# Performance work log

Measured on AMD Instinct MI355X. Metric: run time of the kernel, lower is better.

## Reference

```python
import jax, jax.numpy as jnp
import numpy as np

HEAD_DIM = 128
NUM_Q_HEAD = 32
NUM_KV_HEAD = 8
GROUP_SIZE = 128
EPS = 1e-5
WINDOW = 512
CAP = 50.0
CLIP_L, CLIP_R = -0.01, 1.01
SCALE = 1.0 / np.sqrt(HEAD_DIM)
NEG = -1e9


def group_rmsnorm(x, gamma, gsz, eps):
    # x: [B, S, H]; per-group RMS over contiguous chunks of size gsz, then learned scale
    b, s, h = x.shape
    xg = x.reshape(b, s, h // gsz, gsz)
    rms = jnp.sqrt(jnp.mean(xg * xg, axis=-1, keepdims=True) + eps)
    return (xg / rms).reshape(b, s, h) * gamma


def setup_inputs() -> dict:
    key = jax.random.key(0)
    k1, k2, k3, k4, k5 = jax.random.split(key, 5)
    B, S = 2, 2048
    q = jax.random.normal(k1, (B, S, NUM_Q_HEAD, HEAD_DIM), dtype=jnp.float32)
    k = jax.random.normal(k2, (B, S, NUM_KV_HEAD, HEAD_DIM), dtype=jnp.float32)
    v = jax.random.normal(k3, (B, S, NUM_KV_HEAD, HEAD_DIM), dtype=jnp.float32)
    # GroupRMSNorm weights ~ U(init_range) = U(-1, 1)
    gamma_q = jax.random.uniform(k4, (NUM_Q_HEAD * HEAD_DIM,), dtype=jnp.float32, minval=-1.0, maxval=1.0)
    gamma_k = jax.random.uniform(k5, (NUM_KV_HEAD * HEAD_DIM,), dtype=jnp.float32, minval=-1.0, maxval=1.0)
    return {"q": q, "k": k, "v": v, "gamma_q": gamma_q, "gamma_k": gamma_k}


def reference(q, k, v, gamma_q, gamma_k):
    B, Sq, Hq, D = q.shape
    Sk, Hkv = k.shape[1], k.shape[2]
    # QK GroupRMSNorm on flattened hidden dim
    qn = group_rmsnorm(q.reshape(B, Sq, Hq * D), gamma_q, GROUP_SIZE, EPS).reshape(B, Sq, Hq, D)
    kn = group_rmsnorm(k.reshape(B, Sk, Hkv * D), gamma_k, GROUP_SIZE, EPS).reshape(B, Sk, Hkv, D)
    # GQA: repeat_interleave kv heads to match q heads
    rep = Hq // Hkv
    kr = jnp.repeat(kn, rep, axis=2)
    vr = jnp.repeat(v, rep, axis=2)
    # scores: [B, H, Sq, Sk]
    logits = jnp.einsum('bqhd,bkhd->bhqk', qn, kr) * SCALE
    # softmax capping (temperature path skipped when cap is set)
    logits = jnp.tanh(logits / CAP) * CAP
    # causal + sliding-window mask (aligned at sequence end)
    i = jnp.arange(Sq)[:, None]
    j = jnp.arange(Sk)[None, :]
    pos = i + (Sk - Sq)
    allowed = (j <= pos) & (pos - j <= WINDOW)
    logits = jnp.where(allowed, logits, NEG)
    probs = jax.nn.softmax(logits.astype(jnp.float32), axis=-1)
    # softmax clipping: clamp(probs * (r - l) + l, 0, 1)
    probs = jnp.clip(probs * (CLIP_R - CLIP_L) + CLIP_L, 0.0, 1.0)
    # output: [B, Sq, H, D]
    o = jnp.einsum('bhqk,bkhd->bqhd', probs.astype(q.dtype), vr)
    return o
```

## Files before the change

kernel.cpp:

```cpp
#include <hip/hip_runtime.h>

#define SEQ     2048
#define NQH     32
#define NKV     8
#define HD      128
#define WINDOW  512
#define QT      64
#define EPS_F   1e-5f
#define CQ2     0.12752981793f
#define PSTR    72

#define KN_OFF  0ull
#define VT_OFF  8388608ull

#define ROWPAT(r, hg) ((((r) & 3) + 8 * ((r) >> 2)) + 4 * (hg))

#define ASYNC_BAR() asm volatile("s_waitcnt vmcnt(0)\n\ts_barrier" ::: "memory")
#define LGKM_BAR()  asm volatile("s_waitcnt lgkmcnt(0)\n\ts_barrier" ::: "memory")

using bf16x8 = __attribute__((ext_vector_type(8))) __bf16;
using f32x16 = __attribute__((ext_vector_type(16))) float;

__device__ __forceinline__ void dma16(const void* g, void* l) {
    __builtin_amdgcn_global_load_lds(
        (const __attribute__((address_space(1))) unsigned int*)g,
        (__attribute__((address_space(3))) unsigned int*)l, 16, 0, 0);
}

__global__ __launch_bounds__(256)
void prep(const float* __restrict__ k, const float* __restrict__ v,
          const float* __restrict__ gk,
          __bf16* __restrict__ kn, __bf16* __restrict__ vt)
{
    __shared__ __align__(16) __bf16 sT[HD * 72];
    const int blk = blockIdx.x;
    const int tid = threadIdx.x;
    if (blk < 512) {
        const int l16  = tid & 15;
        const int rsub = tid >> 4;
        #pragma unroll
        for (int it = 0; it < 4; it++) {
            const int row = blk * 64 + it * 16 + rsub;
            const float* src = k + (size_t)row * HD + l16 * 8;
            const float* g   = gk + (row & 7) * HD + l16 * 8;
            float4 a  = *(const float4*)(src);
            float4 b4 = *(const float4*)(src + 4);
            float ss = a.x*a.x + a.y*a.y + a.z*a.z + a.w*a.w
                     + b4.x*b4.x + b4.y*b4.y + b4.z*b4.z + b4.w*b4.w;
            ss += __shfl_xor(ss, 1); ss += __shfl_xor(ss, 2);
            ss += __shfl_xor(ss, 4); ss += __shfl_xor(ss, 8);
            const float rs = rsqrtf(ss * (1.f / 128.f) + EPS_F);
            float4 g0 = *(const float4*)(g);
            float4 g1 = *(const float4*)(g + 4);
            bf16x8 o;
            o[0] = (__bf16)(a.x  * rs * g0.x);  o[1] = (__bf16)(a.y  * rs * g0.y);
            o[2] = (__bf16)(a.z  * rs * g0.z);  o[3] = (__bf16)(a.w  * rs * g0.w);
            o[4] = (__bf16)(b4.x * rs * g1.x);  o[5] = (__bf16)(b4.y * rs * g1.y);
            o[6] = (__bf16)(b4.z * rs * g1.z);  o[7] = (__bf16)(b4.w * rs * g1.w);
            *(bf16x8*)(kn + (size_t)row * HD + l16 * 8) = o;
        }
    } else {
        const int blk2 = blk - 512;
        const int st  = blk2 & 31;
        const int kvh = (blk2 >> 5) & 7;
        const int b   = blk2 >> 8;
        const int s0  = st * 64;
        {
            const int r  = tid >> 2;
            const int q4 = tid & 3;
            const float* src = v + ((size_t)(b * SEQ + s0 + r) * NKV + kvh) * HD;
            #pragma unroll
            for (int u = 0; u < 8; u++) {
                const int d0 = q4 * 4 + u * 16;
                float4 x = *(const float4*)(src + d0);
                sT[(d0 + 0) * 72 + r] = (__bf16)x.x;
                sT[(d0 + 1) * 72 + r] = (__bf16)x.y;
                sT[(d0 + 2) * 72 + r] = (__bf16)x.z;
                sT[(d0 + 3) * 72 + r] = (__bf16)x.w;
            }
        }
        __syncthreads();
        {
            const int c     = tid & 7;
            const int dbase = tid >> 3;
            __bf16* dst = vt + ((size_t)(b * NKV + kvh) * HD) * SEQ + s0;
            #pragma unroll
            for (int i = 0; i < 4; i++) {
                const int d = dbase + i * 32;
                bf16x8 w = *(const bf16x8*)&sT[d * 72 + c * 8];
                *(bf16x8*)(dst + (size_t)d * SEQ + c * 8) = w;
            }
        }
    }
}

__global__ __launch_bounds__(256, 2)
void swa_main(const float* __restrict__ q, const __bf16* __restrict__ kn,
              const __bf16* __restrict__ vt, const float* __restrict__ gq,
              float* __restrict__ out)
{
    __shared__ __align__(16) __bf16 sKV[2][QT * HD];
    __shared__ __align__(16) __bf16 sP[QT * PSTR];
    __shared__ float sLp[2][QT];
    __shared__ float sInvL[QT];

    const int wg   = blockIdx.x;
    const int qt   = wg & 31;
    const int h    = (wg >> 5) & 31;
    const int b    = wg >> 10;
    const int kvh  = h >> 2;
    const int i0   = qt * QT;
    const int tid  = threadIdx.x;
    const int lane = tid & 63;
    const int wave = tid >> 6;
    const int mhalf = wave & 1;
    const int nhalf = wave >> 1;
    const int m    = lane & 31;
    const int hg   = lane >> 5;

    const char* k_src[4];  const char* v_src[4];
    int kq_off[4];  int v_off[4];
    {
        const char* kn_head = (const char*)kn + ((size_t)b * SEQ * NKV + kvh) * 256;
        const char* vt_head = (const char*)vt + ((size_t)(b * NKV + kvh) * HD) * (SEQ * 2);
        #pragma unroll
        for (int i = 0; i < 4; i++) {
            const int chunk = wave * 4 + i;
            {
                const int r    = chunk * 4 + (lane >> 4);
                const int cpos = lane & 15;
                const int c    = (cpos & 8) | ((cpos ^ r) & 7);
                k_src[i]  = kn_head + (size_t)r * (NKV * HD * 2) + c * 16;
                kq_off[i] = chunk * 1024;
            }
            {
                const int r    = chunk * 8 + (lane >> 3);
                const int cpos = lane & 7;
                const int c    = cpos ^ (r & 7);
                v_src[i] = vt_head + (size_t)r * (SEQ * 2) + c * 16;
                v_off[i] = chunk * 1024;
            }
        }
    }

    const int t_lo   = (i0 >= WINDOW ? (i0 - WINDOW) : 0) >> 6;
    const int t_hi   = i0 >> 6;
    const int ttbias = t_hi - 8;
    const int krow   = nhalf * 32 + m;

    {
        const size_t ko = (size_t)t_lo * 64 * (NKV * HD * 2);
        const int p0 = (t_lo - ttbias) & 1;
        #pragma unroll
        for (int i = 0; i < 4; i++) dma16(k_src[i] + ko, (char*)&sKV[p0][0] + kq_off[i]);
    }

    bf16x8 qf[8];
    {
        const int qrow = i0 + mhalf * 32 + m;
        const float* qp = q + ((size_t)(b * SEQ + qrow) * NQH + h) * HD;
        float4 qb[16];
        float ss = 0.0f;
        #pragma unroll
        for (int kf = 0; kf < 8; kf++) {
            const int d0 = kf * 16 + hg * 8;
            float4 a  = *(const float4*)(qp + d0);
            float4 b4 = *(const float4*)(qp + d0 + 4);
            qb[kf * 2] = a; qb[kf * 2 + 1] = b4;
            ss += a.x*a.x + a.y*a.y + a.z*a.z + a.w*a.w
                + b4.x*b4.x + b4.y*b4.y + b4.z*b4.z + b4.w*b4.w;
        }
        ss += __shfl_xor(ss, 32);
        const float rs = rsqrtf(ss * (1.f / 128.f) + EPS_F) * CQ2;
        const float* gp = gq + h * HD;
        #pragma unroll
        for (int kf = 0; kf < 8; kf++) {
            const int d0 = kf * 16 + hg * 8;
            float4 g0 = *(const float4*)(gp + d0);
            float4 g1 = *(const float4*)(gp + d0 + 4);
            bf16x8 f;
            f[0] = (__bf16)(qb[kf*2].x   * rs * g0.x);
            f[1] = (__bf16)(qb[kf*2].y   * rs * g0.y);
            f[2] = (__bf16)(qb[kf*2].z   * rs * g0.z);
            f[3] = (__bf16)(qb[kf*2].w   * rs * g0.w);
            f[4] = (__bf16)(qb[kf*2+1].x * rs * g1.x);
            f[5] = (__bf16)(qb[kf*2+1].y * rs * g1.y);
            f[6] = (__bf16)(qb[kf*2+1].z * rs * g1.z);
            f[7] = (__bf16)(qb[kf*2+1].w * rs * g1.w);
            qf[kf] = f;
        }
    }

    float lacc[16];
    #pragma unroll
    for (int i = 0; i < 16; i++) lacc[i] = 0.f;
    bf16x8 ec[9][2];

    #pragma unroll
    for (int tt = 0; tt < 9; tt++) {
        const int t = ttbias + tt;
        if (t >= t_lo) {
            ASYNC_BAR();
            const __bf16* kb = &sKV[tt & 1][0];
            bf16x8 bk[8];
            #pragma unroll
            for (int kf = 0; kf < 8; kf++) {
                const int cc  = kf * 2 + hg;
                const int pos = (cc & 8) | ((cc ^ krow) & 7);
                bk[kf] = *(const bf16x8*)(kb + krow * HD + pos * 8);
            }
            if (t < t_hi) {
                const size_t ko = (size_t)(t + 1) * 64 * (NKV * HD * 2);
                #pragma unroll
                for (int i = 0; i < 4; i++)
                    dma16(k_src[i] + ko, (char*)&sKV[(tt + 1) & 1][0] + kq_off[i]);
            }
            f32x16 c;
            #pragma unroll
            for (int i = 0; i < 16; i++) c[i] = 0.f;
            #pragma unroll
            for (int kf = 0; kf < 8; kf++)
                c = __builtin_amdgcn_mfma_f32_32x32x16_bf16(qf[kf], bk[kf], c, 0, 0, 0);

            const bool do_mask = (t == t_hi) || (t == t_lo && i0 >= WINDOW);
            const int kj = t * 64 + krow;
            float e[16];
            #pragma unroll
            for (int r = 0; r < 16; r++) {
                float ev = __builtin_amdgcn_exp2f(c[r]);
                if (do_mask) {
                    const int qi = i0 + mhalf * 32 + ROWPAT(r, hg);
                    ev = ((unsigned)(qi - kj) <= WINDOW) ? ev : 0.f;
                }
                lacc[r] += ev;
                e[r] = ev;
            }
            bf16x8 p0v, p1v;
            #pragma unroll
            for (int j = 0; j < 8; j++) { p0v[j] = (__bf16)e[j]; p1v[j] = (__bf16)e[8 + j]; }
            ec[tt][0] = p0v;  ec[tt][1] = p1v;
        }
    }

    #pragma unroll
    for (int r = 0; r < 16; r++) {
        float l = lacc[r];
        l += __shfl_xor(l, 1);  l += __shfl_xor(l, 2);  l += __shfl_xor(l, 4);
        l += __shfl_xor(l, 8);  l += __shfl_xor(l, 16);
        lacc[r] = l;
    }
    if (m == 0) {
        #pragma unroll
        for (int r = 0; r < 16; r++)
            sLp[nhalf][mhalf * 32 + ROWPAT(r, hg)] = lacc[r];
    }
    __syncthreads();
    if (tid < QT) sInvL[tid] = __builtin_amdgcn_rcpf(sLp[0][tid] + sLp[1][tid]);
    __syncthreads();

    float ar[16];
    #pragma unroll
    for (int r = 0; r < 16; r++) ar[r] = 1.02f * sInvL[mhalf * 32 + ROWPAT(r, hg)];

    {
        const size_t vo = (size_t)t_lo * 128;
        const int p0 = (t_lo - ttbias) & 1;
        #pragma unroll
        for (int i = 0; i < 4; i++) dma16(v_src[i] + vo, (char*)&sKV[p0][0] + v_off[i]);
    }

    f32x16 o0, o1;
    #pragma unroll
    for (int i = 0; i < 16; i++) { o0[i] = 0.f; o1[i] = 0.f; }

    #pragma unroll
    for (int tt = 0; tt < 9; tt++) {
        const int t = ttbias + tt;
        if (t >= t_lo) {
            ASYNC_BAR();
            #pragma unroll
            for (int half = 0; half < 2; half++) {
                #pragma unroll
                for (int j = 0; j < 8; j++) {
                    const int r = half * 8 + j;
                    const float ee = (float)ec[tt][half][j];
                    const float f = fminf(fmaxf(fmaf(ee, ar[r], -0.01f), 0.f), 1.f);
                    sP[(mhalf * 32 + ROWPAT(r, hg)) * PSTR + krow] = (__bf16)f;
                }
            }
            LGKM_BAR();
            const __bf16* vb = &sKV[tt & 1][0];
            bf16x8 pa[4], vf0[4], vf1[4];
            #pragma unroll
            for (int kf = 0; kf < 4; kf++) {
                pa[kf] = *(const bf16x8*)&sP[(mhalf * 32 + m) * PSTR + kf * 16 + hg * 8];
                const int cc = kf * 2 + hg;
                const int row0 = nhalf * 64 + m;
                const int row1 = nhalf * 64 + 32 + m;
                vf0[kf] = *(const bf16x8*)(vb + row0 * 64 + ((cc ^ row0) & 7) * 8);
                vf1[kf] = *(const bf16x8*)(vb + row1 * 64 + ((cc ^ row1) & 7) * 8);
            }
            if (t < t_hi) {
                const size_t vo = (size_t)(t + 1) * 128;
                #pragma unroll
                for (int i = 0; i < 4; i++)
                    dma16(v_src[i] + vo, (char*)&sKV[(tt + 1) & 1][0] + v_off[i]);
            }
            #pragma unroll
            for (int kf = 0; kf < 4; kf++) {
                o0 = __builtin_amdgcn_mfma_f32_32x32x16_bf16(pa[kf], vf0[kf], o0, 0, 0, 0);
                o1 = __builtin_amdgcn_mfma_f32_32x32x16_bf16(pa[kf], vf1[kf], o1, 0, 0, 0);
            }
        }
    }

    #pragma unroll
    for (int r = 0; r < 16; r++) {
        const int row = i0 + mhalf * 32 + ROWPAT(r, hg);
        float* op = out + ((size_t)(b * SEQ + row) * NQH + h) * HD + nhalf * 64 + m;
        op[0]  = o0[r];
        op[32] = o1[r];
    }
}

extern "C" void kernel_launch(void* const* d_in, const int* in_sizes, int n_in,
                              void* d_out, int out_size, void* d_ws, size_t ws_size,
                              hipStream_t stream) {
    const float* q  = (const float*)d_in[0];
    const float* k  = (const float*)d_in[1];
    const float* v  = (const float*)d_in[2];
    const float* gq = (const float*)d_in[3];
    const float* gk = (const float*)d_in[4];
    float* out = (float*)d_out;

    __bf16* kn = (__bf16*)((char*)d_ws + KN_OFF);
    __bf16* vt = (__bf16*)((char*)d_ws + VT_OFF);

    prep<<<1024, 256, 0, stream>>>(k, v, gk, kn, vt);
    swa_main<<<2 * NQH * (SEQ / QT), 256, 0, stream>>>(q, kn, vt, gq, out);
}
```

Baseline: 217.3 us.

## Triple-buffer K/V tiles with two-deep async prefetch and partial vmcnt waits

Grows the shared K/V staging from two to three buffers and issues global-to-LDS loads two tiles ahead. The barrier waits only for the older tile (vmcnt(4)), so one tile's load stays in flight during compute. The V prefetch is also moved earlier, between the row-sum reduction barriers, to overlap with the 1/l computation. The extra buffer adds 16KB of LDS per block, which may lower occupancy at 2 blocks per CU, and correctness relies on each wave's vmcnt ordering.

```diff
diff --git a/kernel.cpp b/kernel.cpp
--- a/kernel.cpp
+++ b/kernel.cpp
@@ -15,7 +15,8 @@
 
 #define ROWPAT(r, hg) ((((r) & 3) + 8 * ((r) >> 2)) + 4 * (hg))
 
-#define ASYNC_BAR() asm volatile("s_waitcnt vmcnt(0)\n\ts_barrier" ::: "memory")
+#define WAIT_BAR_4() asm volatile("s_waitcnt vmcnt(4)\n\ts_barrier" ::: "memory")
+#define WAIT_BAR_0() asm volatile("s_waitcnt vmcnt(0)\n\ts_barrier" ::: "memory")
 #define LGKM_BAR()  asm volatile("s_waitcnt lgkmcnt(0)\n\ts_barrier" ::: "memory")
 
 using bf16x8 = __attribute__((ext_vector_type(8))) __bf16;
@@ -99,7 +100,7 @@
               const __bf16* __restrict__ vt, const float* __restrict__ gq,
               float* __restrict__ out)
 {
-    __shared__ __align__(16) __bf16 sKV[2][QT * HD];
+    __shared__ __align__(16) __bf16 sKV[3][QT * HD];
     __shared__ __align__(16) __bf16 sP[QT * PSTR];
     __shared__ float sLp[2][QT];
     __shared__ float sInvL[QT];
@@ -147,12 +148,18 @@
     const int t_hi   = i0 >> 6;
     const int ttbias = t_hi - 8;
     const int krow   = nhalf * 32 + m;
+    const size_t kstride = (size_t)64 * (NKV * HD * 2);
 
     {
-        const size_t ko = (size_t)t_lo * 64 * (NKV * HD * 2);
-        const int p0 = (t_lo - ttbias) & 1;
-        #pragma unroll
-        for (int i = 0; i < 4; i++) dma16(k_src[i] + ko, (char*)&sKV[p0][0] + kq_off[i]);
+        const size_t ko = (size_t)t_lo * kstride;
+        char* dst0 = (char*)&sKV[t_lo % 3][0];
+        #pragma unroll
+        for (int i = 0; i < 4; i++) dma16(k_src[i] + ko, dst0 + kq_off[i]);
+        if (t_lo < t_hi) {
+            char* dst1 = (char*)&sKV[(t_lo + 1) % 3][0];
+            #pragma unroll
+            for (int i = 0; i < 4; i++) dma16(k_src[i] + ko + kstride, dst1 + kq_off[i]);
+        }
     }
 
     bf16x8 qf[8];
@@ -200,8 +207,8 @@
     for (int tt = 0; tt < 9; tt++) {
         const int t = ttbias + tt;
         if (t >= t_lo) {
-            ASYNC_BAR();
-            const __bf16* kb = &sKV[tt & 1][0];
+            if (t < t_hi) { WAIT_BAR_4(); } else { WAIT_BAR_0(); }
+            const __bf16* kb = &sKV[t % 3][0];
             bf16x8 bk[8];
             #pragma unroll
             for (int kf = 0; kf < 8; kf++) {
@@ -209,11 +216,11 @@
                 const int pos = (cc & 8) | ((cc ^ krow) & 7);
                 bk[kf] = *(const bf16x8*)(kb + krow * HD + pos * 8);
             }
-            if (t < t_hi) {
-                const size_t ko = (size_t)(t + 1) * 64 * (NKV * HD * 2);
+            if (t + 2 <= t_hi) {
+                const size_t ko = (size_t)(t + 2) * kstride;
+                char* dstp = (char*)&sKV[(t + 2) % 3][0];
                 #pragma unroll
-                for (int i = 0; i < 4; i++)
-                    dma16(k_src[i] + ko, (char*)&sKV[(tt + 1) & 1][0] + kq_off[i]);
+                for (int i = 0; i < 4; i++) dma16(k_src[i] + ko, dstp + kq_off[i]);
             }
             f32x16 c;
             #pragma unroll
@@ -254,20 +261,24 @@
         for (int r = 0; r < 16; r++)
             sLp[nhalf][mhalf * 32 + ROWPAT(r, hg)] = lacc[r];
     }
-    __syncthreads();
-    if (tid < QT) sInvL[tid] = __builtin_amdgcn_rcpf(sLp[0][tid] + sLp[1][tid]);
-    __syncthreads();
-
-    float ar[16];
-    #pragma unroll
-    for (int r = 0; r < 16; r++) ar[r] = 1.02f * sInvL[mhalf * 32 + ROWPAT(r, hg)];
-
+    LGKM_BAR();
     {
         const size_t vo = (size_t)t_lo * 128;
-        const int p0 = (t_lo - ttbias) & 1;
-        #pragma unroll
-        for (int i = 0; i < 4; i++) dma16(v_src[i] + vo, (char*)&sKV[p0][0] + v_off[i]);
-    }
+        char* dst0 = (char*)&sKV[t_lo % 3][0];
+        #pragma unroll
+        for (int i = 0; i < 4; i++) dma16(v_src[i] + vo, dst0 + v_off[i]);
+        if (t_lo < t_hi) {
+            char* dst1 = (char*)&sKV[(t_lo + 1) % 3][0];
+            #pragma unroll
+            for (int i = 0; i < 4; i++) dma16(v_src[i] + vo + 128, dst1 + v_off[i]);
+        }
+    }
+    if (tid < QT) sInvL[tid] = __builtin_amdgcn_rcpf(sLp[0][tid] + sLp[1][tid]);
+    LGKM_BAR();
+
+    float ar[16];
+    #pragma unroll
+    for (int r = 0; r < 16; r++) ar[r] = 1.02f * sInvL[mhalf * 32 + ROWPAT(r, hg)];
 
     f32x16 o0, o1;
     #pragma unroll
@@ -277,7 +288,7 @@
     for (int tt = 0; tt < 9; tt++) {
         const int t = ttbias + tt;
         if (t >= t_lo) {
-            ASYNC_BAR();
+            if (t < t_hi) { WAIT_BAR_4(); } else { WAIT_BAR_0(); }
             #pragma unroll
             for (int half = 0; half < 2; half++) {
                 #pragma unroll
@@ -289,7 +300,7 @@
                 }
             }
             LGKM_BAR();
-            const __bf16* vb = &sKV[tt & 1][0];
+            const __bf16* vb = &sKV[t % 3][0];
             bf16x8 pa[4], vf0[4], vf1[4];
             #pragma unroll
             for (int kf = 0; kf < 4; kf++) {
@@ -300,11 +311,11 @@
                 vf0[kf] = *(const bf16x8*)(vb + row0 * 64 + ((cc ^ row0) & 7) * 8);
                 vf1[kf] = *(const bf16x8*)(vb + row1 * 64 + ((cc ^ row1) & 7) * 8);
             }
-            if (t < t_hi) {
-                const size_t vo = (size_t)(t + 1) * 128;
+            if (t + 2 <= t_hi) {
+                const size_t vo = (size_t)(t + 2) * 128;
+                char* dstp = (char*)&sKV[(t + 2) % 3][0];
                 #pragma unroll
-                for (int i = 0; i < 4; i++)
-                    dma16(v_src[i] + vo, (char*)&sKV[(tt + 1) & 1][0] + v_off[i]);
+                for (int i = 0; i < 4; i++) dma16(v_src[i] + vo, dstp + v_off[i]);
             }
             #pragma unroll
             for (int kf = 0; kf < 4; kf++) {
```

After: 213.1 us, median of 3. About the same (-1.9%).
